# Kernel optimization log

Measured on AMD Instinct MI355X. Metric: run time of the kernel, lower is better.

## Reference

```python
import jax, jax.numpy as jnp
import numpy as np

B, N, FD, FI, IOU = 4, 512, 256, 128, 1

def _linear_params(key, out_f, in_f):
    k1, k2 = jax.random.split(key)
    bound = 1.0 / np.sqrt(in_f)
    W = jax.random.uniform(k1, (out_f, in_f), jnp.float32, -bound, bound)
    b = jax.random.uniform(k2, (out_f,), jnp.float32, -bound, bound)
    return W, b

def setup_inputs() -> dict:
    key = jax.random.key(0)
    ks = jax.random.split(key, 10)
    node_features = jax.random.normal(ks[0], (B, N, FD), jnp.float32)
    supress_mat = (jax.random.uniform(ks[1], (B, N, N)) < 0.5).astype(jnp.float32)
    pos_emb_mat = jax.random.normal(ks[2], (B, N, N, 2), jnp.float32)
    Wp, bp = _linear_params(ks[3], FI, 2)        # pos_linear
    Wi, bi = _linear_params(ks[4], FI, FD)       # linear_in
    Wo, bo = _linear_params(ks[5], FI, FD)       # linear_out
    We1, be1 = _linear_params(ks[6], FI, FI)     # edge_layers[0]
    We2, be2 = _linear_params(ks[7], IOU, FI)    # edge_layers[2]
    Wn1, bn1 = _linear_params(ks[8], FD, IOU)    # node_layers[0]
    Wn2, bn2 = _linear_params(ks[9], FD, FD)     # node_layers[2]
    return dict(node_features=node_features, supress_mat=supress_mat, pos_emb_mat=pos_emb_mat,
                Wp=Wp, bp=bp, Wi=Wi, bi=bi, Wo=Wo, bo=bo,
                We1=We1, be1=be1, We2=We2, be2=be2,
                Wn1=Wn1, bn1=bn1, Wn2=Wn2, bn2=bn2)

def reference(node_features, supress_mat, pos_emb_mat,
              Wp, bp, Wi, bi, Wo, bo, We1, be1, We2, be2, Wn1, bn1, Wn2, bn2):
    # node_features: [B,N,FD]; supress_mat: [B,N,N]; pos_emb_mat: [B,N,N,2]
    nf_in = jnp.einsum('bnd,fd->bnf', node_features, Wi) + bi     # [B,N,FI]
    nf_out = jnp.einsum('bnd,fd->bnf', node_features, Wo) + bo    # [B,N,FI]
    edge_emb = jnp.einsum('bijc,fc->bijf', pos_emb_mat, Wp) + bp  # [B,N,N,FI]
    # broadcast diff: [B,N,1,FI] - [B,1,N,FI] + [B,N,N,FI]
    e = nf_in[:, :, None, :] - nf_out[:, None, :, :] + edge_emb
    e = jnp.einsum('bijf,gf->bijg', e, We1) + be1
    e = jax.nn.gelu(e, approximate=False)
    e = jnp.einsum('bijf,gf->bijg', e, We2) + be2                 # [B,N,N,IOU]
    e = e * supress_mat[..., None]
    node_max = jnp.max(e, axis=1)                                 # [B,N,IOU]
    h = jax.nn.relu(jnp.einsum('bni,di->bnd', node_max, Wn1) + bn1)
    h = jax.nn.relu(jnp.einsum('bnd,ed->bne', h, Wn2) + bn2)
    return h
```

## Files before the change

### kernel.cpp

```cpp
#include <hip/hip_runtime.h>
#include <hip/hip_bf16.h>

#define NN 512
#define FD 256
#define FI 128

typedef __attribute__((ext_vector_type(2))) float f2;

#define OFF_AIN   0
#define OFF_D     262144
#define OFF_UINT  524288
#define OFF_UOUTT 557056
#define OFF_COEF  589824
#define OFF_BIAS  590336
#define OFF_PART  590592
#define OFF_WN2T  623360

__device__ __forceinline__ f2 pk_fma(f2 a, f2 b, f2 c) {
    return __builtin_elementwise_fma(a, b, c);
}

__device__ __forceinline__ f2 gelu2(f2 x) {
    f2 x2 = x * x;
    f2 s  = pk_fma(x2, (f2)(0.10294325f), (f2)(2.3022083f));
    f2 zs = x * s;
    f2 e;
    e.x = __builtin_amdgcn_exp2f(zs.x);
    e.y = __builtin_amdgcn_exp2f(zs.y);
    f2 ep = e + (f2)(1.0f);
    f2 r;
    r.x = __builtin_amdgcn_rcpf(ep.x);
    r.y = __builtin_amdgcn_rcpf(ep.y);
    return pk_fma(-x, r, x);
}

__global__ __launch_bounds__(256) void prep_kernel(
    const float* __restrict__ Wp,  const float* __restrict__ bp,
    const float* __restrict__ Wi,  const float* __restrict__ bi,
    const float* __restrict__ Wo,  const float* __restrict__ bo,
    const float* __restrict__ We1, const float* __restrict__ be1,
    const float* __restrict__ We2, const float* __restrict__ Wn2,
    float* ws)
{
    int bidx = blockIdx.x;
    int d = threadIdx.x;
    if (bidx >= 256) {
        int e = bidx - 256;
        float v = Wn2[e * FD + d];
        ws[OFF_WN2T + (d >> 2) * (FD * 4) + e * 4 + (d & 3)] = v;
        return;
    }
    int io = bidx >> 7, g = bidx & 127;
    const float* W = io ? Wo : Wi;
    const float* wrow = We1 + g * FI;
    float acc = 0.f;
    for (int f = 0; f < FI; ++f)
        acc = __fmaf_rn(wrow[f], W[f * FD + d], acc);
    ws[(io ? OFF_UOUTT : OFF_UINT) + d * FI + g] = acc;

    if (bidx == 0 && d < FI) {
        const float* wr = We1 + d * FI;
        float a0 = 0.f, a1 = 0.f, abi = 0.f, abo = 0.f;
        for (int f = 0; f < FI; ++f) {
            float w = wr[f];
            a0  = __fmaf_rn(w, Wp[f * 2 + 0], a0);
            a1  = __fmaf_rn(w, Wp[f * 2 + 1], a1);
            abi = __fmaf_rn(w, bi[f] + bp[f], abi);
            abo = __fmaf_rn(w, bo[f], abo);
        }
        int gq = d >> 2, k = d & 3;
        ws[OFF_COEF + gq * 16 + k]     = a0;
        ws[OFF_COEF + gq * 16 + 4 + k] = a1;
        ws[OFF_COEF + gq * 16 + 8 + k] = We2[d];
        ws[OFF_BIAS + d]       = abi + be1[d];
        ws[OFF_BIAS + 128 + d] = abo;
    }
}

__global__ __launch_bounds__(256) void proj_kernel(
    const float* __restrict__ x, float* ws)
{
    __shared__ __align__(16) float xs[4][FD];
    int t  = threadIdx.x;
    int nb = blockIdx.x * 4;
    ((float4*)xs)[t] = ((const float4*)(x + nb * FD))[t];
    __syncthreads();

    int lane = t & 63, gq = lane & 31, io = lane >> 5;
    int n0 = t >> 6;
    const float4* U4 = (const float4*)(ws + (io ? OFF_UOUTT : OFF_UINT));
    float4 bias = ((const float4*)(ws + OFF_BIAS + io * 128))[gq];
    float4 a0 = {0.f, 0.f, 0.f, 0.f};
    #pragma unroll 8
    for (int d = 0; d < FD; ++d) {
        float4 u = U4[d * 32 + gq];
        float x0 = xs[n0][d];
        a0.x = __fmaf_rn(u.x, x0, a0.x);
        a0.y = __fmaf_rn(u.y, x0, a0.y);
        a0.z = __fmaf_rn(u.z, x0, a0.z);
        a0.w = __fmaf_rn(u.w, x0, a0.w);
    }
    float sgn = io ? -1.f : 1.f;
    float4 v0;
    v0.x = sgn * (a0.x + bias.x); v0.y = sgn * (a0.y + bias.y);
    v0.z = sgn * (a0.z + bias.z); v0.w = sgn * (a0.w + bias.w);
    float* dst = ws + (io ? OFF_D : OFF_AIN);
    *(float4*)(dst + (nb + n0) * FI + gq * 4) = v0;
}

__global__ __launch_bounds__(512) void edge_kernel(
    const float* __restrict__ pos, const float* __restrict__ sup,
    const float* __restrict__ Ain, const float* __restrict__ Dmat,
    const float* __restrict__ coef, const float* __restrict__ be2p,
    float* __restrict__ part)
{
    __shared__ __align__(16) float sD[32 * 128];
    __shared__ __align__(16) float sA[32 * 128];
    __shared__ unsigned short sList[1024];
    __shared__ int smax[32];
    __shared__ int scnt;

    int tile = blockIdx.x;
    int ir = tile & 15, jt = (tile >> 4) & 15, b = tile >> 8;
    int tid = threadIdx.x;
    int lane = tid & 63;

    const float4* Dg4 = (const float4*)(Dmat + (b * NN + jt * 32) * FI);
    #pragma unroll
    for (int k = 0; k < 2; ++k) {
        int s = tid + k * 512;
        float4 v = Dg4[s];
        int r = s >> 5, c = (s & 31) * 4;
        *(float4*)(sD + r * 128 + (c ^ ((r & 31) << 2))) = v;
    }
    const float4* Ag4 = (const float4*)(Ain + (b * NN + ir * 32) * FI);
    #pragma unroll
    for (int k = 0; k < 2; ++k) {
        int s = tid + k * 512;
        float4 v = Ag4[s];
        int r = s >> 5, c = (s & 31) * 4;
        *(float4*)(sA + r * 128 + (c ^ ((r & 31) << 2))) = v;
    }
    if (tid < 32) smax[tid] = 0;
    if (tid == 0) scnt = 0;
    __syncthreads();

    const float* S = sup + (size_t)(b * NN + ir * 32) * NN + jt * 32;
    #pragma unroll
    for (int k = 0; k < 2; ++k) {
        int s = tid + k * 512;
        int i_l = s >> 5, j_l = s & 31;
        bool act = (S[i_l * NN + j_l] != 0.f);
        unsigned long long mask = __ballot(act);
        int wbase = 0;
        if (lane == 0 && mask) wbase = atomicAdd(&scnt, (int)__popcll(mask));
        wbase = __shfl(wbase, 0);
        if (act) {
            int prefix = (int)__popcll(mask & ((1ull << lane) - 1ull));
            sList[wbase + prefix] = (unsigned short)s;
        }
    }
    __syncthreads();

    int cnt = scnt;
    float be2 = *be2p;
    const float2* pos2 = (const float2*)pos;

    for (int r = tid; r < cnt; r += 512) {
        int e = (int)sList[r];
        int i_l = e >> 5, j_l = e & 31;
        float2 pp = pos2[(size_t)(b * NN + ir * 32 + i_l) * NN + jt * 32 + j_l];
        const float* Ar = sA + i_l * 128;
        const float* Dr = sD + j_l * 128;
        int aswz = i_l << 2;
        int dswz = j_l << 2;
        f2 px = {pp.x, pp.x}, py = {pp.y, pp.y};
        f2 z01 = {0.f, 0.f}, z23 = {0.f, 0.f};
        #pragma unroll 4
        for (int gq = 0; gq < 32; ++gq) {
            float4 a  = *(const float4*)(Ar + ((gq * 4) ^ aswz));
            float4 d  = *(const float4*)(Dr + ((gq * 4) ^ dswz));
            float4 w0 = *(const float4*)(coef + gq * 16);
            float4 w1 = *(const float4*)(coef + gq * 16 + 4);
            float4 vv = *(const float4*)(coef + gq * 16 + 8);
            f2 a01 = {a.x, a.y}, a23 = {a.z, a.w};
            f2 d01 = {d.x, d.y}, d23 = {d.z, d.w};
            f2 w001 = {w0.x, w0.y}, w023 = {w0.z, w0.w};
            f2 w101 = {w1.x, w1.y}, w123 = {w1.z, w1.w};
            f2 v01 = {vv.x, vv.y}, v23 = {vv.z, vv.w};
            f2 y01 = pk_fma(w101, py, pk_fma(w001, px, a01 + d01));
            f2 y23 = pk_fma(w123, py, pk_fma(w023, px, a23 + d23));
            z01 = pk_fma(v01, gelu2(y01), z01);
            z23 = pk_fma(v23, gelu2(y23), z23);
        }
        float z = (z01.x + z01.y) + (z23.x + z23.y);
        atomicMax(&smax[j_l], __float_as_int(z + be2));
    }
    __syncthreads();
    if (tid < 32)
        part[tile * 32 + tid] = __int_as_float(smax[tid]);
}

__global__ __launch_bounds__(256) void final_kernel(
    const float* __restrict__ Wn1, const float* __restrict__ bn1,
    const float* __restrict__ wtx, const float* __restrict__ bn2,
    const float* __restrict__ part, float* __restrict__ out)
{
    __shared__ float red[4][17];
    __shared__ float nm[4];
    __shared__ __align__(16) float h1[4][FD];
    int nb = blockIdx.x * 4;
    int b  = nb >> 9;
    int j0 = nb & 511;
    int jt = j0 >> 5, jl0 = j0 & 31;
    int t = threadIdx.x;
    if (t < 64) {
        int k = t & 3, ir = t >> 2;
        red[k][ir] = part[(((b * 16 + jt) * 16) + ir) * 32 + jl0 + k];
    }
    __syncthreads();
    if (t < 4) {
        float m2 = red[t][0];
        #pragma unroll
        for (int q = 1; q < 16; ++q) m2 = fmaxf(m2, red[t][q]);
        nm[t] = m2;
    }
    __syncthreads();
    {
        float wv = Wn1[t];
        float bv = bn1[t];
        #pragma unroll
        for (int n = 0; n < 4; ++n)
            h1[n][t] = fmaxf(0.f, __fmaf_rn(nm[n], wv, bv));
    }
    __syncthreads();
    float acc[4] = {0.f, 0.f, 0.f, 0.f};
    const float4* WX = (const float4*)wtx;
    #pragma unroll 4
    for (int d4 = 0; d4 < FD / 4; ++d4) {
        float4 w = WX[d4 * FD + t];
        #pragma unroll
        for (int n = 0; n < 4; ++n) {
            float4 hv = *(const float4*)(&h1[n][d4 * 4]);
            acc[n] = __fmaf_rn(w.x, hv.x, acc[n]);
            acc[n] = __fmaf_rn(w.y, hv.y, acc[n]);
            acc[n] = __fmaf_rn(w.z, hv.z, acc[n]);
            acc[n] = __fmaf_rn(w.w, hv.w, acc[n]);
        }
    }
    float bb = bn2[t];
    #pragma unroll
    for (int n = 0; n < 4; ++n)
        out[(size_t)(nb + n) * FD + t] = fmaxf(0.f, acc[n] + bb);
}

extern "C" void kernel_launch(void* const* d_in, const int* in_sizes, int n_in,
                              void* d_out, int out_size, void* d_ws, size_t ws_size,
                              hipStream_t stream) {
    (void)in_sizes; (void)n_in; (void)out_size; (void)ws_size;
    const float* node = (const float*)d_in[0];
    const float* sup  = (const float*)d_in[1];
    const float* pos  = (const float*)d_in[2];
    const float* Wp   = (const float*)d_in[3];
    const float* bp   = (const float*)d_in[4];
    const float* Wi   = (const float*)d_in[5];
    const float* bi   = (const float*)d_in[6];
    const float* Wo   = (const float*)d_in[7];
    const float* bo   = (const float*)d_in[8];
    const float* We1  = (const float*)d_in[9];
    const float* be1  = (const float*)d_in[10];
    const float* We2  = (const float*)d_in[11];
    const float* be2  = (const float*)d_in[12];
    const float* Wn1  = (const float*)d_in[13];
    const float* bn1  = (const float*)d_in[14];
    const float* Wn2  = (const float*)d_in[15];
    const float* bn2  = (const float*)d_in[16];
    float* ws  = (float*)d_ws;
    float* out = (float*)d_out;

    prep_kernel<<<512, 256, 0, stream>>>(Wp, bp, Wi, bi, Wo, bo,
                                         We1, be1, We2, Wn2, ws);
    proj_kernel<<<512, 256, 0, stream>>>(node, ws);
    edge_kernel<<<1024, 512, 0, stream>>>(pos, sup, ws + OFF_AIN, ws + OFF_D,
                                          ws + OFF_COEF, be2, ws + OFF_PART);
    final_kernel<<<512, 256, 0, stream>>>(Wn1, bn1, ws + OFF_WN2T, bn2,
                                          ws + OFF_PART, out);
}
```

Baseline: 65.27 us.

## Register-block projection kernel over 8 nodes with packed FMA

The projection kernel now handles 8 nodes per block instead of 4. Each thread owns one output feature and accumulates all 8 nodes, reusing each weight load 8 times and using packed 2-wide FMAs with float4 reads from shared memory. This is meant to cut redundant global weight traffic and instruction count in the small projection GEMM. The trade-offs are half as many blocks (less parallelism), more registers per thread, and scalar strided weight loads and output stores in place of float4 accesses.

After: 69.19 us. 1.06x slower.

```diff
diff --git a/kernel.cpp b/kernel.cpp
--- a/kernel.cpp
+++ b/kernel.cpp
@@ -80,32 +80,41 @@
 __global__ __launch_bounds__(256) void proj_kernel(
     const float* __restrict__ x, float* ws)
 {
-    __shared__ __align__(16) float xs[4][FD];
+    __shared__ __align__(16) float xs[8][FD];
     int t  = threadIdx.x;
-    int nb = blockIdx.x * 4;
-    ((float4*)xs)[t] = ((const float4*)(x + nb * FD))[t];
-    __syncthreads();
-
-    int lane = t & 63, gq = lane & 31, io = lane >> 5;
-    int n0 = t >> 6;
-    const float4* U4 = (const float4*)(ws + (io ? OFF_UOUTT : OFF_UINT));
-    float4 bias = ((const float4*)(ws + OFF_BIAS + io * 128))[gq];
-    float4 a0 = {0.f, 0.f, 0.f, 0.f};
-    #pragma unroll 8
-    for (int d = 0; d < FD; ++d) {
-        float4 u = U4[d * 32 + gq];
-        float x0 = xs[n0][d];
-        a0.x = __fmaf_rn(u.x, x0, a0.x);
-        a0.y = __fmaf_rn(u.y, x0, a0.y);
-        a0.z = __fmaf_rn(u.z, x0, a0.z);
-        a0.w = __fmaf_rn(u.w, x0, a0.w);
-    }
+    int nb = blockIdx.x * 8;
+    ((float4*)xs)[t]       = ((const float4*)(x + nb * FD))[t];
+    ((float4*)xs)[t + 256] = ((const float4*)(x + nb * FD))[t + 256];
+    __syncthreads();
+
+    int io = t >> 7, g = t & 127;
+    const float* UT = ws + (io ? OFF_UOUTT : OFF_UINT) + g;
+    float bias = ws[OFF_BIAS + io * 128 + g];
+    f2 acc[8];
+    #pragma unroll
+    for (int n = 0; n < 8; ++n) acc[n] = (f2)(0.f);
+
+    #pragma unroll 2
+    for (int d4 = 0; d4 < FD; d4 += 4) {
+        float u0 = UT[(d4 + 0) * FI];
+        float u1 = UT[(d4 + 1) * FI];
+        float u2 = UT[(d4 + 2) * FI];
+        float u3 = UT[(d4 + 3) * FI];
+        f2 u01 = {u0, u1}, u23 = {u2, u3};
+        #pragma unroll
+        for (int n = 0; n < 8; ++n) {
+            float4 xv = *(const float4*)(&xs[n][d4]);
+            f2 x01 = {xv.x, xv.y}, x23 = {xv.z, xv.w};
+            acc[n] = pk_fma(u01, x01, acc[n]);
+            acc[n] = pk_fma(u23, x23, acc[n]);
+        }
+    }
+
     float sgn = io ? -1.f : 1.f;
-    float4 v0;
-    v0.x = sgn * (a0.x + bias.x); v0.y = sgn * (a0.y + bias.y);
-    v0.z = sgn * (a0.z + bias.z); v0.w = sgn * (a0.w + bias.w);
     float* dst = ws + (io ? OFF_D : OFF_AIN);
-    *(float4*)(dst + (nb + n0) * FI + gq * 4) = v0;
+    #pragma unroll
+    for (int n = 0; n < 8; ++n)
+        dst[(nb + n) * FI + g] = sgn * (acc[n].x + acc[n].y + bias);
 }
 
 __global__ __launch_bounds__(512) void edge_kernel(
@@ -280,7 +289,7 @@
 
     prep_kernel<<<512, 256, 0, stream>>>(Wp, bp, Wi, bi, Wo, bo,
                                          We1, be1, We2, Wn2, ws);
-    proj_kernel<<<512, 256, 0, stream>>>(node, ws);
+    proj_kernel<<<256, 256, 0, stream>>>(node, ws);
     edge_kernel<<<1024, 512, 0, stream>>>(pos, sup, ws + OFF_AIN, ws + OFF_D,
                                           ws + OFF_COEF, be2, ws + OFF_PART);
     final_kernel<<<512, 256, 0, stream>>>(Wn1, bn1, ws + OFF_WN2T, bn2,
```
